# Kernel optimization log

Hardware: AMD Instinct MI355X
Metric: run time of the kernel (lower is better)

The kernel has to match this reference:

```python
import jax, jax.numpy as jnp
import numpy as np

EPS = 1e-09

def setup_inputs() -> dict:
    key = jax.random.key(0)
    k1, k2 = jax.random.split(key)
    N, C = 65536, 1024
    pred = jax.random.normal(k1, (N, C), dtype=jnp.float32)
    target = jax.random.randint(k2, (N,), 0, C, dtype=jnp.int64)
    return {"pred": pred, "target": target}

def reference(pred, target):
    # Faithful to the torch module: softmax over dim=0 (across the batch dim)
    p = jax.nn.softmax(pred, axis=0) + EPS  # epsilon added before BOTH log terms
    C = pred.shape[1]
    tar = jax.nn.one_hot(target, C, dtype=pred.dtype)  # [N, C]
    # per-row BCE with log base 2, mean over classes
    bce = tar * jnp.log2(p) + (1.0 - tar) * jnp.log2(1.0 - p)
    loss = -jnp.mean(bce, axis=1)  # [N]
    return jnp.mean(loss)
```

## Files before the change

kernel.cpp:

```cpp
#include <hip/hip_runtime.h>
#include <math.h>

static constexpr int N = 65536;
static constexpr int C = 1024;
static constexpr float EPS = 1e-9f;


template <int RPB>
__global__ __launch_bounds__(256) void colsum_partial_kernel(
    const float* __restrict__ pred, const int* __restrict__ tgt,
    float* __restrict__ partial, float* __restrict__ sxArr,
    int* __restrict__ counter) {
    const int tid  = threadIdx.x;
    const int row0 = blockIdx.x * RPB;
    if (blockIdx.x == 0 && tid == 0) *counter = 0;

    __shared__ int tgt_lds[RPB];
    if (tid < RPB) tgt_lds[tid] = tgt[row0 + tid];
    __syncthreads();

    const float4* __restrict__ p4 =
        reinterpret_cast<const float4*>(pred) + (size_t)row0 * (C / 4) + tid;

    float a0 = 0.f, a1 = 0.f, a2 = 0.f, a3 = 0.f;
    float sx = 0.f;
#pragma unroll 1
    for (int b = 0; b < RPB / 8; ++b) {
        float4 v0 = p4[0 * (C / 4)];
        float4 v1 = p4[1 * (C / 4)];
        float4 v2 = p4[2 * (C / 4)];
        float4 v3 = p4[3 * (C / 4)];
        float4 v4 = p4[4 * (C / 4)];
        float4 v5 = p4[5 * (C / 4)];
        float4 v6 = p4[6 * (C / 4)];
        float4 v7 = p4[7 * (C / 4)];
        p4 += 8 * (C / 4);
        __builtin_amdgcn_sched_barrier(0);

#pragma unroll
        for (int r = 0; r < 8; ++r) {
            const int tc = tgt_lds[b * 8 + r];
            if ((tc >> 2) == tid) {
                const float4 v = (r == 0) ? v0 : (r == 1) ? v1 : (r == 2) ? v2
                               : (r == 3) ? v3 : (r == 4) ? v4 : (r == 5) ? v5
                               : (r == 6) ? v6 : v7;
                const int sel = tc & 3;
                sx += (sel == 0) ? v.x : (sel == 1) ? v.y : (sel == 2) ? v.z : v.w;
            }
        }

        a0 += __expf(v0.x) + __expf(v1.x) + __expf(v2.x) + __expf(v3.x)
            + __expf(v4.x) + __expf(v5.x) + __expf(v6.x) + __expf(v7.x);
        a1 += __expf(v0.y) + __expf(v1.y) + __expf(v2.y) + __expf(v3.y)
            + __expf(v4.y) + __expf(v5.y) + __expf(v6.y) + __expf(v7.y);
        a2 += __expf(v0.z) + __expf(v1.z) + __expf(v2.z) + __expf(v3.z)
            + __expf(v4.z) + __expf(v5.z) + __expf(v6.z) + __expf(v7.z);
        a3 += __expf(v0.w) + __expf(v1.w) + __expf(v2.w) + __expf(v3.w)
            + __expf(v4.w) + __expf(v5.w) + __expf(v6.w) + __expf(v7.w);
    }

    reinterpret_cast<float4*>(partial + (size_t)blockIdx.x * C)[tid] =
        make_float4(a0, a1, a2, a3);

#pragma unroll
    for (int off = 32; off > 0; off >>= 1)
        sx += __shfl_down(sx, off, 64);
    __shared__ float wsum[4];
    if ((tid & 63) == 0) wsum[tid >> 6] = sx;
    __syncthreads();
    if (tid == 0)
        sxArr[blockIdx.x] = wsum[0] + wsum[1] + wsum[2] + wsum[3];
}

__global__ __launch_bounds__(256) void colreduce_kernel(
    const float* __restrict__ partial, float* __restrict__ logS, int RB) {
    const int t  = threadIdx.x;
    const int cp = t & 7;
    const int r0 = t >> 3;
    const int c0 = blockIdx.x * 16;
    const int eighth = RB / 8;

    const float2* __restrict__ p2 =
        reinterpret_cast<const float2*>(partial) + (c0 >> 1) + cp;

    float2 a[8];
#pragma unroll
    for (int j = 0; j < 8; ++j) a[j] = make_float2(0.f, 0.f);
    for (int r = r0; r < eighth; r += 32) {
#pragma unroll
        for (int j = 0; j < 8; ++j) {
            const float2 v = p2[(size_t)(r + j * eighth) * (C / 2)];
            a[j].x += v.x;
            a[j].y += v.y;
        }
    }
    float2 s;
    s.x = ((a[0].x + a[1].x) + (a[2].x + a[3].x)) + ((a[4].x + a[5].x) + (a[6].x + a[7].x));
    s.y = ((a[0].y + a[1].y) + (a[2].y + a[3].y)) + ((a[4].y + a[5].y) + (a[6].y + a[7].y));
#pragma unroll
    for (int off = 8; off <= 32; off <<= 1) {
        s.x += __shfl_xor(s.x, off, 64);
        s.y += __shfl_xor(s.y, off, 64);
    }
    __shared__ float2 wred[4][8];
    if ((t & 63) < 8) wred[t >> 6][cp] = s;
    __syncthreads();
    if (t < 8) {
        const float vx = wred[0][t].x + wred[1][t].x + wred[2][t].x + wred[3][t].x;
        const float vy = wred[0][t].y + wred[1][t].y + wred[2][t].y + wred[3][t].y;
        logS[c0 + 2 * t]     = log2f(vx);
        logS[c0 + 2 * t + 1] = log2f(vy);
    }
}

__global__ __launch_bounds__(256) void gather_finalize_kernel(
    const int* __restrict__ tgt, const float* __restrict__ logS,
    const float* __restrict__ sxArr, float* __restrict__ gArr,
    int* __restrict__ counter, float* __restrict__ out, int RB) {
    const int t = threadIdx.x;
    float v = logS[tgt[blockIdx.x * 256 + t]];
#pragma unroll
    for (int off = 32; off > 0; off >>= 1)
        v += __shfl_down(v, off, 64);
    __shared__ float wsum[4];
    if ((t & 63) == 0) wsum[t >> 6] = v;
    __syncthreads();

    __shared__ int last;
    if (t == 0) {
        gArr[blockIdx.x] = wsum[0] + wsum[1] + wsum[2] + wsum[3];
        __threadfence();
        const int old = __hip_atomic_fetch_add(counter, 1, __ATOMIC_ACQ_REL,
                                               __HIP_MEMORY_SCOPE_AGENT);
        last = (old == (int)gridDim.x - 1) ? 1 : 0;
    }
    __syncthreads();
    if (!last) return;

    float gl = __hip_atomic_load(&gArr[t], __ATOMIC_RELAXED,
                                 __HIP_MEMORY_SCOPE_AGENT);
    float sx = 0.f;
    for (int i = t; i < RB; i += 256) sx += sxArr[i];
#pragma unroll
    for (int off = 32; off > 0; off >>= 1) {
        gl += __shfl_down(gl, off, 64);
        sx += __shfl_down(sx, off, 64);
    }
    __shared__ float r1[4], r2[4];
    if ((t & 63) == 0) { r1[t >> 6] = gl; r2[t >> 6] = sx; }
    __syncthreads();
    if (t == 0) {
        const double LOG2E = 1.4426950408889634;
        const double SumLogS = (double)(r1[0] + r1[1] + r1[2] + r1[3]);
        const double SumX    = (double)(r2[0] + r2[1] + r2[2] + r2[3]);
        const double termA   = -LOG2E * (double)C * (1.0 + (double)N * (double)EPS);
        const double total   = termA + LOG2E * SumX - SumLogS;
        out[0] = (float)(-total / ((double)N * (double)C));
    }
}

extern "C" void kernel_launch(void* const* d_in, const int* in_sizes, int n_in,
                              void* d_out, int out_size, void* d_ws, size_t ws_size,
                              hipStream_t stream) {
    const float* pred = (const float*)d_in[0];
    const int*   tgt  = (const int*)d_in[1];
    float* wsf     = (float*)d_ws;
    float* logS    = wsf;
    int*   counter = (int*)(wsf + 1024);
    float* sxArr   = wsf + 1088;
    float* gArr    = wsf + 3200;
    float* partial = wsf + 4096;
    const size_t base_bytes = 4096 * sizeof(float);

    int RB = 2048;
    while (RB > 512 && base_bytes + (size_t)RB * C * sizeof(float) > ws_size)
        RB >>= 1;

    if (RB >= 2048)
        colsum_partial_kernel<32><<<2048, 256, 0, stream>>>(pred, tgt, partial, sxArr, counter);
    else if (RB == 1024)
        colsum_partial_kernel<64><<<1024, 256, 0, stream>>>(pred, tgt, partial, sxArr, counter);
    else
        colsum_partial_kernel<128><<<512, 256, 0, stream>>>(pred, tgt, partial, sxArr, counter);

    colreduce_kernel<<<64, 256, 0, stream>>>(partial, logS, RB);
    gather_finalize_kernel<<<256, 256, 0, stream>>>(tgt, logS, sxArr, gArr,
                                                    counter, (float*)d_out, RB);
}
```

Measured before the change: 65.03 us.

## Move target-logit gather to finalize kernel and software-pipeline colsum loads

The colsum kernel no longer loads targets into LDS or does the per-row target-selection compare and block reduction. The target logit is instead gathered directly from pred in the finalize kernel and combined with logS per row. The colsum loop is also software-pipelined, issuing the next 8 row loads before the exps on the current ones, which raises register use. The gather adds 65536 scattered 4-byte reads from the 256MB input, which will mostly miss the cache.

```diff
diff --git a/kernel.cpp b/kernel.cpp
--- a/kernel.cpp
+++ b/kernel.cpp
@@ -7,69 +7,64 @@
 
 
 template <int RPB>
-__global__ __launch_bounds__(256) void colsum_partial_kernel(
-    const float* __restrict__ pred, const int* __restrict__ tgt,
-    float* __restrict__ partial, float* __restrict__ sxArr,
+__global__ __launch_bounds__(256) void colsum_kernel(
+    const float* __restrict__ pred, float* __restrict__ partial,
     int* __restrict__ counter) {
-    const int tid  = threadIdx.x;
-    const int row0 = blockIdx.x * RPB;
+    const int tid = threadIdx.x;
     if (blockIdx.x == 0 && tid == 0) *counter = 0;
 
-    __shared__ int tgt_lds[RPB];
-    if (tid < RPB) tgt_lds[tid] = tgt[row0 + tid];
-    __syncthreads();
-
     const float4* __restrict__ p4 =
-        reinterpret_cast<const float4*>(pred) + (size_t)row0 * (C / 4) + tid;
+        reinterpret_cast<const float4*>(pred) +
+        (size_t)blockIdx.x * RPB * (C / 4) + tid;
 
     float a0 = 0.f, a1 = 0.f, a2 = 0.f, a3 = 0.f;
-    float sx = 0.f;
+
+    float4 v0 = p4[0 * (C / 4)];
+    float4 v1 = p4[1 * (C / 4)];
+    float4 v2 = p4[2 * (C / 4)];
+    float4 v3 = p4[3 * (C / 4)];
+    float4 v4 = p4[4 * (C / 4)];
+    float4 v5 = p4[5 * (C / 4)];
+    float4 v6 = p4[6 * (C / 4)];
+    float4 v7 = p4[7 * (C / 4)];
+    p4 += 8 * (C / 4);
+
 #pragma unroll 1
-    for (int b = 0; b < RPB / 8; ++b) {
-        float4 v0 = p4[0 * (C / 4)];
-        float4 v1 = p4[1 * (C / 4)];
-        float4 v2 = p4[2 * (C / 4)];
-        float4 v3 = p4[3 * (C / 4)];
-        float4 v4 = p4[4 * (C / 4)];
-        float4 v5 = p4[5 * (C / 4)];
-        float4 v6 = p4[6 * (C / 4)];
-        float4 v7 = p4[7 * (C / 4)];
+    for (int b = 0; b < RPB / 8 - 1; ++b) {
+        float4 w0 = p4[0 * (C / 4)];
+        float4 w1 = p4[1 * (C / 4)];
+        float4 w2 = p4[2 * (C / 4)];
+        float4 w3 = p4[3 * (C / 4)];
+        float4 w4 = p4[4 * (C / 4)];
+        float4 w5 = p4[5 * (C / 4)];
+        float4 w6 = p4[6 * (C / 4)];
+        float4 w7 = p4[7 * (C / 4)];
         p4 += 8 * (C / 4);
         __builtin_amdgcn_sched_barrier(0);
 
-#pragma unroll
-        for (int r = 0; r < 8; ++r) {
-            const int tc = tgt_lds[b * 8 + r];
-            if ((tc >> 2) == tid) {
-                const float4 v = (r == 0) ? v0 : (r == 1) ? v1 : (r == 2) ? v2
-                               : (r == 3) ? v3 : (r == 4) ? v4 : (r == 5) ? v5
-                               : (r == 6) ? v6 : v7;
-                const int sel = tc & 3;
-                sx += (sel == 0) ? v.x : (sel == 1) ? v.y : (sel == 2) ? v.z : v.w;
-            }
-        }
+        a0 += __expf(v0.x); a1 += __expf(v0.y); a2 += __expf(v0.z); a3 += __expf(v0.w);
+        a0 += __expf(v1.x); a1 += __expf(v1.y); a2 += __expf(v1.z); a3 += __expf(v1.w);
+        a0 += __expf(v2.x); a1 += __expf(v2.y); a2 += __expf(v2.z); a3 += __expf(v2.w);
+        a0 += __expf(v3.x); a1 += __expf(v3.y); a2 += __expf(v3.z); a3 += __expf(v3.w);
+        a0 += __expf(v4.x); a1 += __expf(v4.y); a2 += __expf(v4.z); a3 += __expf(v4.w);
+        a0 += __expf(v5.x); a1 += __expf(v5.y); a2 += __expf(v5.z); a3 += __expf(v5.w);
+        a0 += __expf(v6.x); a1 += __expf(v6.y); a2 += __expf(v6.z); a3 += __expf(v6.w);
+        a0 += __expf(v7.x); a1 += __expf(v7.y); a2 += __expf(v7.z); a3 += __expf(v7.w);
 
-        a0 += __expf(v0.x) + __expf(v1.x) + __expf(v2.x) + __expf(v3.x)
-            + __expf(v4.x) + __expf(v5.x) + __expf(v6.x) + __expf(v7.x);
-        a1 += __expf(v0.y) + __expf(v1.y) + __expf(v2.y) + __expf(v3.y)
-            + __expf(v4.y) + __expf(v5.y) + __expf(v6.y) + __expf(v7.y);
-        a2 += __expf(v0.z) + __expf(v1.z) + __expf(v2.z) + __expf(v3.z)
-            + __expf(v4.z) + __expf(v5.z) + __expf(v6.z) + __expf(v7.z);
-        a3 += __expf(v0.w) + __expf(v1.w) + __expf(v2.w) + __expf(v3.w)
-            + __expf(v4.w) + __expf(v5.w) + __expf(v6.w) + __expf(v7.w);
+        v0 = w0; v1 = w1; v2 = w2; v3 = w3;
+        v4 = w4; v5 = w5; v6 = w6; v7 = w7;
     }
+    a0 += __expf(v0.x); a1 += __expf(v0.y); a2 += __expf(v0.z); a3 += __expf(v0.w);
+    a0 += __expf(v1.x); a1 += __expf(v1.y); a2 += __expf(v1.z); a3 += __expf(v1.w);
+    a0 += __expf(v2.x); a1 += __expf(v2.y); a2 += __expf(v2.z); a3 += __expf(v2.w);
+    a0 += __expf(v3.x); a1 += __expf(v3.y); a2 += __expf(v3.z); a3 += __expf(v3.w);
+    a0 += __expf(v4.x); a1 += __expf(v4.y); a2 += __expf(v4.z); a3 += __expf(v4.w);
+    a0 += __expf(v5.x); a1 += __expf(v5.y); a2 += __expf(v5.z); a3 += __expf(v5.w);
+    a0 += __expf(v6.x); a1 += __expf(v6.y); a2 += __expf(v6.z); a3 += __expf(v6.w);
+    a0 += __expf(v7.x); a1 += __expf(v7.y); a2 += __expf(v7.z); a3 += __expf(v7.w);
 
     reinterpret_cast<float4*>(partial + (size_t)blockIdx.x * C)[tid] =
         make_float4(a0, a1, a2, a3);
-
-#pragma unroll
-    for (int off = 32; off > 0; off >>= 1)
-        sx += __shfl_down(sx, off, 64);
-    __shared__ float wsum[4];
-    if ((tid & 63) == 0) wsum[tid >> 6] = sx;
-    __syncthreads();
-    if (tid == 0)
-        sxArr[blockIdx.x] = wsum[0] + wsum[1] + wsum[2] + wsum[3];
 }
 
 __global__ __launch_bounds__(256) void colreduce_kernel(
@@ -113,12 +108,16 @@
     }
 }
 
-__global__ __launch_bounds__(256) void gather_finalize_kernel(
-    const int* __restrict__ tgt, const float* __restrict__ logS,
-    const float* __restrict__ sxArr, float* __restrict__ gArr,
-    int* __restrict__ counter, float* __restrict__ out, int RB) {
+__global__ __launch_bounds__(256) void target_finalize_kernel(
+    const int* __restrict__ tgt, const float* __restrict__ pred,
+    const float* __restrict__ logS, float* __restrict__ gArr,
+    int* __restrict__ counter, float* __restrict__ out) {
     const int t = threadIdx.x;
-    float v = logS[tgt[blockIdx.x * 256 + t]];
+    const int n = blockIdx.x * 256 + t;
+    const int c = tgt[n];
+    const float x = pred[((size_t)n << 10) + c];
+    const float LOG2E_F = 1.4426950408889634f;
+    float v = LOG2E_F * x - logS[c];
 #pragma unroll
     for (int off = 32; off > 0; off >>= 1)
         v += __shfl_down(v, off, 64);
@@ -139,22 +138,17 @@
 
     float gl = __hip_atomic_load(&gArr[t], __ATOMIC_RELAXED,
                                  __HIP_MEMORY_SCOPE_AGENT);
-    float sx = 0.f;
-    for (int i = t; i < RB; i += 256) sx += sxArr[i];
 #pragma unroll
-    for (int off = 32; off > 0; off >>= 1) {
+    for (int off = 32; off > 0; off >>= 1)
         gl += __shfl_down(gl, off, 64);
-        sx += __shfl_down(sx, off, 64);
-    }
-    __shared__ float r1[4], r2[4];
-    if ((t & 63) == 0) { r1[t >> 6] = gl; r2[t >> 6] = sx; }
+    __shared__ float r1[4];
+    if ((t & 63) == 0) r1[t >> 6] = gl;
     __syncthreads();
     if (t == 0) {
         const double LOG2E = 1.4426950408889634;
-        const double SumLogS = (double)(r1[0] + r1[1] + r1[2] + r1[3]);
-        const double SumX    = (double)(r2[0] + r2[1] + r2[2] + r2[3]);
-        const double termA   = -LOG2E * (double)C * (1.0 + (double)N * (double)EPS);
-        const double total   = termA + LOG2E * SumX - SumLogS;
+        const double SumContrib = (double)(r1[0] + r1[1] + r1[2] + r1[3]);
+        const double termA = -LOG2E * (double)C * (1.0 + (double)N * (double)EPS);
+        const double total = termA + SumContrib;
         out[0] = (float)(-total / ((double)N * (double)C));
     }
 }
@@ -167,8 +161,7 @@
     float* wsf     = (float*)d_ws;
     float* logS    = wsf;
     int*   counter = (int*)(wsf + 1024);
-    float* sxArr   = wsf + 1088;
-    float* gArr    = wsf + 3200;
+    float* gArr    = wsf + 1088;
     float* partial = wsf + 4096;
     const size_t base_bytes = 4096 * sizeof(float);
 
@@ -177,13 +170,13 @@
         RB >>= 1;
 
     if (RB >= 2048)
-        colsum_partial_kernel<32><<<2048, 256, 0, stream>>>(pred, tgt, partial, sxArr, counter);
+        colsum_kernel<32><<<2048, 256, 0, stream>>>(pred, partial, counter);
     else if (RB == 1024)
-        colsum_partial_kernel<64><<<1024, 256, 0, stream>>>(pred, tgt, partial, sxArr, counter);
+        colsum_kernel<64><<<1024, 256, 0, stream>>>(pred, partial, counter);
     else
-        colsum_partial_kernel<128><<<512, 256, 0, stream>>>(pred, tgt, partial, sxArr, counter);
+        colsum_kernel<128><<<512, 256, 0, stream>>>(pred, partial, counter);
 
     colreduce_kernel<<<64, 256, 0, stream>>>(partial, logS, RB);
-    gather_finalize_kernel<<<256, 256, 0, stream>>>(tgt, logS, sxArr, gArr,
-                                                    counter, (float*)d_out, RB);
+    target_finalize_kernel<<<256, 256, 0, stream>>>(tgt, pred, logS, gArr,
+                                                    counter, (float*)d_out);
 }
```

Result: faster. 62.78 us (-3.5%).
